# Kernel tuning notes

Measured on AMD Instinct MI355X. Metric: run time of the kernel, lower is better.

## Reference

```python
import jax, jax.numpy as jnp
import numpy as np

POS_W = 1.0
ANG_W = 1.0
WID_W = 1.0
N = 1048560  # predictions (divisible by 17)
M = 8388480  # total GT grasps = sum(arange(N) % 17)


def setup_inputs() -> dict:
    key = jax.random.key(0)
    k1, k2 = jax.random.split(key)
    pred = jax.random.normal(k1, (N, 6), dtype=jnp.float32)
    all_targets = jax.random.normal(k2, (M, 6), dtype=jnp.float32)
    # ragged counts in [0, 16]; sum == M exactly
    target_counts = (jnp.arange(N, dtype=jnp.int64) % 17)
    return {"pred": pred, "all_targets": all_targets, "target_counts": target_counts}


def _smooth_l1(x):
    a = jnp.abs(x)
    return jnp.where(a < 1.0, 0.5 * x * x, a - 0.5)


def reference(pred, all_targets, target_counts):
    n = pred.shape[0]
    m = all_targets.shape[0]
    # segment id for each GT row (contiguous slices, order of target_counts)
    seg = jnp.repeat(jnp.arange(n), target_counts, total_repeat_length=m)  # (M,)
    p = pred[seg]  # (M,6) gathered predictions
    dp = p[:, :2] - all_targets[:, :2]
    da = p[:, 2:4] - all_targets[:, 2:4]
    dw = p[:, 4] - all_targets[:, 4]
    dist = (POS_W * jnp.sum(dp * dp, axis=-1)
            + ANG_W * jnp.sum(da * da, axis=-1)
            + WID_W * dw * dw)  # (M,)
    # ragged argmin per segment (first occurrence, like torch.argmin)
    min_d = jax.ops.segment_min(dist, seg, num_segments=n)  # (N,)
    row = jnp.arange(m)
    cand = jnp.where(dist == min_d[seg], row, m)
    arg = jax.ops.segment_min(cand, seg, num_segments=n)  # (N,) global row idx or m
    has = target_counts > 0
    gt = all_targets[jnp.where(has, jnp.clip(arg, 0, m - 1), 0)]  # (N,6)
    # fused per-prediction loss against the closest GT
    loss_pos = jnp.sum(_smooth_l1(pred[:, :2] - gt[:, :2]), axis=-1)
    loss_ang = jnp.sum(jnp.abs(pred[:, 2:4] - gt[:, 2:4]), axis=-1)
    loss_wid = _smooth_l1(pred[:, 4] - gt[:, 4])
    losses = jnp.where(has, POS_W * loss_pos + ANG_W * loss_ang + WID_W * loss_wid, 0.0)
    return jnp.mean(losses)  # reduction='mean'
```

## Files before the change

### kernel.cpp

```cpp
#include <hip/hip_runtime.h>
#include <math.h>
#include <stdint.h>

#define POS_W 1.0f
#define ANG_W 1.0f
#define WID_W 1.0f
#define CHUNK 1024
#define F4PT 6

__device__ __forceinline__ float smooth_l1(float x) {
    float a = fabsf(x);
    return a < 1.0f ? 0.5f * x * x : a - 0.5f;
}

__device__ __forceinline__ void bar_lds() {
    asm volatile("s_waitcnt lgkmcnt(0)" ::: "memory");
    __builtin_amdgcn_s_barrier();
    __builtin_amdgcn_sched_barrier(0);
}

__global__ void k_block_sums(const int* __restrict__ counts, int stride, int n,
                             int* __restrict__ blockSums) {
    int i = blockIdx.x * 256 + threadIdx.x;
    int c = (i < n) ? counts[(long long)i * stride] : 0;
    for (int off = 32; off > 0; off >>= 1) c += __shfl_down(c, off, 64);
    __shared__ int sdata[4];
    int lane = threadIdx.x & 63, wave = threadIdx.x >> 6;
    if (lane == 0) sdata[wave] = c;
    __syncthreads();
    if (threadIdx.x == 0)
        blockSums[blockIdx.x] = sdata[0] + sdata[1] + sdata[2] + sdata[3];
}

__global__ __launch_bounds__(256) void k_loss(
    const float* __restrict__ pred, const float* __restrict__ tgt,
    const int* __restrict__ counts, int stride, int n, int mrows,
    const int* __restrict__ blockSums, float invN, float* __restrict__ out) {
    __shared__ float4 ch4[CHUNK * 3 / 2 + 1];
    __shared__ int wsum[4];
    __shared__ int wpre[4];
    __shared__ float fs[4];

    int t = threadIdx.x;
    int lane = t & 63, wave = t >> 6;
    int b = blockIdx.x;
    int i = b * 256 + t;
    int c = (i < n) ? counts[(long long)i * stride] : 0;

    int pre = 0;
    for (int j = t; j < b; j += 256) pre += blockSums[j];

    int incl = c;
#pragma unroll
    for (int d = 1; d < 64; d <<= 1) {
        int v = __shfl_up(incl, d, 64);
        if (lane >= d) incl += v;
    }
    for (int o = 32; o > 0; o >>= 1) pre += __shfl_down(pre, o, 64);
    if (lane == 63) wsum[wave] = incl;
    if (lane == 0) wpre[wave] = pre;
    __syncthreads();

    int w0 = wsum[0], w1 = wsum[1], w2 = wsum[2], w3 = wsum[3];
    int waveOff = (wave > 0 ? w0 : 0) + (wave > 1 ? w1 : 0) + (wave > 2 ? w2 : 0);
    int off = waveOff + incl - c;
    int total = w0 + w1 + w2 + w3;
    int winStart = wpre[0] + wpre[1] + wpre[2] + wpre[3];

    bool active = (i < n) && (c > 0);
    float p0 = 0, p1 = 0, p2 = 0, p3 = 0, p4 = 0;
    if (active) {
        const float2* p2p = (const float2*)(pred + (long long)i * 6);
        float2 a = p2p[0], bb = p2p[1], w = p2p[2];
        p0 = a.x; p1 = a.y; p2 = bb.x; p3 = bb.y; p4 = w.x;
    }

    long long winB = (long long)winStart * 24;
    long long alignedB = winB & ~15ll;
    const float4* win4 = (const float4*)((const char*)tgt + alignedB);
    int sh = (int)(winStart & 1);
    int f4maxi = (int)(((long long)mrows * 24 - alignedB) >> 4);

    float best = INFINITY;
    float b0 = 0, b1 = 0, b2 = 0, b3 = 0, b4 = 0;
    const float2* ch2 = (const float2*)ch4;
    float4 rf[F4PT];

    {
        int rows0 = min(CHUNK, total);
        int nF4 = (rows0 * 3 + sh + 1) >> 1;
        int lim = min(nF4, f4maxi);
#pragma unroll
        for (int j = 0; j < F4PT; ++j) {
            int q = t + 256 * j;
            if (q < lim) rf[j] = win4[q];
        }
    }

    for (int base = 0; base < total; base += CHUNK) {
        int rows = min(CHUNK, total - base);
        int nF4c = (rows * 3 + sh + 1) >> 1;
        int qB = (base * 3) >> 1;
        int lim = min(nF4c, f4maxi - qB);
#pragma unroll
        for (int j = 0; j < F4PT; ++j) {
            int q = t + 256 * j;
            if (q < lim) ch4[q] = rf[j];
        }
        bar_lds();
        int nbase = base + CHUNK;
        if (nbase < total) {
            int rowsn = min(CHUNK, total - nbase);
            int nF4n = (rowsn * 3 + sh + 1) >> 1;
            int qBn = (nbase * 3) >> 1;
            int limn = min(nF4n, f4maxi - qBn);
#pragma unroll
            for (int j = 0; j < F4PT; ++j) {
                int q = t + 256 * j;
                if (q < limn) rf[j] = win4[qBn + q];
            }
        }
        if (active) {
            int lo = max(off, base), hi = min(off + c, base + rows);
            for (int rr = lo; rr < hi; ++rr) {
                int l2i = (rr - base) * 3 + sh;
                float2 ga = ch2[l2i], gb = ch2[l2i + 1], gw = ch2[l2i + 2];
                float d0 = p0 - ga.x, d1 = p1 - ga.y;
                float d2 = p2 - gb.x, d3 = p3 - gb.y;
                float d4 = p4 - gw.x;
                float dist = POS_W * (d0 * d0 + d1 * d1) +
                             ANG_W * (d2 * d2 + d3 * d3) + WID_W * d4 * d4;
                if (dist < best) {
                    best = dist;
                    b0 = ga.x; b1 = ga.y; b2 = gb.x; b3 = gb.y; b4 = gw.x;
                }
            }
        }
        bar_lds();
    }

    float loss = 0.0f;
    if (active) {
        loss = POS_W * (smooth_l1(p0 - b0) + smooth_l1(p1 - b1)) +
               ANG_W * (fabsf(p2 - b2) + fabsf(p3 - b3)) +
               WID_W * smooth_l1(p4 - b4);
    }

    for (int o = 32; o > 0; o >>= 1) loss += __shfl_down(loss, o, 64);
    if (lane == 0) fs[wave] = loss;
    __syncthreads();
    if (t == 0) {
        float tot = (fs[0] + fs[1] + fs[2] + fs[3]) * invN;
        atomicAdd(out, tot);
    }
}

extern "C" void kernel_launch(void* const* d_in, const int* in_sizes, int n_in,
                              void* d_out, int out_size, void* d_ws,
                              size_t ws_size, hipStream_t stream) {
    const float* pred = (const float*)d_in[0];
    const float* tgt = (const float*)d_in[1];
    const int* counts = (const int*)d_in[2];
    int n = in_sizes[0] / 6;
    int mrows = in_sizes[1] / 6;
    int stride = (in_sizes[2] == n) ? 1 : 2;
    int nb = (n + 255) / 256;

    int* blockSums = (int*)d_ws;
    float* out = (float*)d_out;

    hipMemsetAsync(d_out, 0, sizeof(float), stream);
    k_block_sums<<<nb, 256, 0, stream>>>(counts, stride, n, blockSums);
    k_loss<<<nb, 256, 0, stream>>>(pred, tgt, counts, stride, n, mrows,
                                   blockSums, 1.0f / n, out);
}
```

Baseline: 361.8 us.

## Stream target chunks directly into double-buffered LDS via global_load_lds

Replaces the register-staged prefetch (global load into registers, then store into one LDS buffer) with direct global-to-LDS loads into two LDS buffers. The next chunk is issued before the current one is consumed, and vmcnt waits order the buffers. This removes the register staging and the LDS write pass, and cuts register pressure. The chunk shrinks to 682 rows so that 16 segments of 64 float4 fit, which means more loop iterations and barriers for each block.

```diff
diff --git a/kernel.cpp b/kernel.cpp
--- a/kernel.cpp
+++ b/kernel.cpp
@@ -5,18 +5,19 @@
 #define POS_W 1.0f
 #define ANG_W 1.0f
 #define WID_W 1.0f
-#define CHUNK 1024
-#define F4PT 6
+#define CHUNK 682
+#define SEGS 16
+#define SEGS_PER_WAVE 4
 
 __device__ __forceinline__ float smooth_l1(float x) {
     float a = fabsf(x);
     return a < 1.0f ? 0.5f * x * x : a - 0.5f;
 }
 
-__device__ __forceinline__ void bar_lds() {
-    asm volatile("s_waitcnt lgkmcnt(0)" ::: "memory");
-    __builtin_amdgcn_s_barrier();
-    __builtin_amdgcn_sched_barrier(0);
+__device__ __forceinline__ void gl_lds16(const float4* g, float4* l) {
+    __builtin_amdgcn_global_load_lds(
+        (const __attribute__((address_space(1))) void*)g,
+        (__attribute__((address_space(3))) void*)l, 16, 0, 0);
 }
 
 __global__ void k_block_sums(const int* __restrict__ counts, int stride, int n,
@@ -36,7 +37,7 @@
     const float* __restrict__ pred, const float* __restrict__ tgt,
     const int* __restrict__ counts, int stride, int n, int mrows,
     const int* __restrict__ blockSums, float invN, float* __restrict__ out) {
-    __shared__ float4 ch4[CHUNK * 3 / 2 + 1];
+    __shared__ float4 bufs[2][SEGS * 64];
     __shared__ int wsum[4];
     __shared__ int wpre[4];
     __shared__ float fs[4];
@@ -77,50 +78,42 @@
 
     long long winB = (long long)winStart * 24;
     long long alignedB = winB & ~15ll;
-    const float4* win4 = (const float4*)((const char*)tgt + alignedB);
+    long long base4 = alignedB >> 4;
     int sh = (int)(winStart & 1);
-    int f4maxi = (int)(((long long)mrows * 24 - alignedB) >> 4);
+    long long f4last = (((long long)mrows * 24) >> 4) - 1;
+    const float4* tgt4 = (const float4*)tgt;
+
+    auto issue_chunk = [&](int bi, int chunkBase) {
+        long long q0 = base4 + (((long long)chunkBase * 3) >> 1);
+#pragma unroll
+        for (int k = 0; k < SEGS_PER_WAVE; ++k) {
+            int seg = wave + 4 * k;
+            long long gi = q0 + seg * 64 + lane;
+            if (gi > f4last) gi = f4last;
+            gl_lds16(tgt4 + gi, &bufs[bi][seg * 64]);
+        }
+    };
 
     float best = INFINITY;
     float b0 = 0, b1 = 0, b2 = 0, b3 = 0, b4 = 0;
-    const float2* ch2 = (const float2*)ch4;
-    float4 rf[F4PT];
 
-    {
-        int rows0 = min(CHUNK, total);
-        int nF4 = (rows0 * 3 + sh + 1) >> 1;
-        int lim = min(nF4, f4maxi);
-#pragma unroll
-        for (int j = 0; j < F4PT; ++j) {
-            int q = t + 256 * j;
-            if (q < lim) rf[j] = win4[q];
-        }
-    }
+    if (total > 0) issue_chunk(0, 0);
 
-    for (int base = 0; base < total; base += CHUNK) {
-        int rows = min(CHUNK, total - base);
-        int nF4c = (rows * 3 + sh + 1) >> 1;
-        int qB = (base * 3) >> 1;
-        int lim = min(nF4c, f4maxi - qB);
-#pragma unroll
-        for (int j = 0; j < F4PT; ++j) {
-            int q = t + 256 * j;
-            if (q < lim) ch4[q] = rf[j];
-        }
-        bar_lds();
+    int cur = 0;
+    for (int base = 0; base < total; base += CHUNK, cur ^= 1) {
         int nbase = base + CHUNK;
         if (nbase < total) {
-            int rowsn = min(CHUNK, total - nbase);
-            int nF4n = (rowsn * 3 + sh + 1) >> 1;
-            int qBn = (nbase * 3) >> 1;
-            int limn = min(nF4n, f4maxi - qBn);
-#pragma unroll
-            for (int j = 0; j < F4PT; ++j) {
-                int q = t + 256 * j;
-                if (q < limn) rf[j] = win4[qBn + q];
-            }
+            issue_chunk(cur ^ 1, nbase);
+            asm volatile("s_waitcnt vmcnt(4)" ::: "memory");
+        } else {
+            asm volatile("s_waitcnt vmcnt(0)" ::: "memory");
         }
+        __builtin_amdgcn_s_barrier();
+        __builtin_amdgcn_sched_barrier(0);
+
         if (active) {
+            int rows = min(CHUNK, total - base);
+            const float2* ch2 = (const float2*)&bufs[cur][0];
             int lo = max(off, base), hi = min(off + c, base + rows);
             for (int rr = lo; rr < hi; ++rr) {
                 int l2i = (rr - base) * 3 + sh;
@@ -136,7 +129,9 @@
                 }
             }
         }
-        bar_lds();
+        asm volatile("s_waitcnt lgkmcnt(0)" ::: "memory");
+        __builtin_amdgcn_s_barrier();
+        __builtin_amdgcn_sched_barrier(0);
     }
 
     float loss = 0.0f;
```

Result: faster. 314.4 us (-13.1%).
